# Optimization experiments

Measured on AMD Instinct MI355X. Metric: run time of the kernel, lower is better.

The kernel has to match this reference:

```python
import jax, jax.numpy as jnp
import numpy as np

KSZ = 1  # kernel_size from init_kwargs


def setup_inputs() -> dict:
    key = jax.random.key(0)
    k1, k2 = jax.random.split(key)
    S, B, H, W = 10, 8, 512, 512
    predicted = jax.random.normal(k1, (S, B, H, W), dtype=jnp.float32)
    target = jax.random.uniform(k2, (B, S, H, W), dtype=jnp.float32)
    mask = jnp.ones((B, S, H, W), dtype=jnp.float32)
    return {"predicted": predicted, "target": target, "mask": mask}


def reference(predicted, target, mask):
    # predicted: [S,B,H,W] -> [B,S,H,W] (torch .permute(1,0,2,3))
    pred = jnp.transpose(predicted, (1, 0, 2, 3))
    # use_weights=False -> weights = ones_like(target); mask unused
    weights = jnp.ones_like(target)
    H, W = target.shape[-2], target.shape[-1]

    # The torch loop does a running strict-< min over shifts (x,y) in row-major
    # order, seeded with the unshifted (0,0) loss. Final selection therefore is
    # the FIRST shift (in order [(0,0)] + loop order) achieving the global min,
    # which is exactly jnp.argmin's first-occurrence tie-breaking.
    shifts = [(0, 0)] + [(x, y) for x in range(-KSZ, KSZ + 1)
                         for y in range(-KSZ, KSZ + 1)]

    pad = jnp.pad(pred, ((0, 0), (0, 0), (KSZ, KSZ), (KSZ, KSZ)))
    valid = jnp.pad(jnp.ones((H, W), dtype=bool),
                    ((KSZ, KSZ), (KSZ, KSZ)))  # in-bounds map

    cands, losses = [], []
    for (x, y) in shifts:
        # candidate at pixel (i,j) is predicted[i+x, j+y]
        c = pad[..., KSZ + x:KSZ + x + H, KSZ + y:KSZ + y + W]
        v = valid[KSZ + x:KSZ + x + H, KSZ + y:KSZ + y + W]
        l = jnp.abs((target - c) * weights)
        losses.append(jnp.where(v, l, jnp.inf))
        cands.append(c)

    cands = jnp.stack(cands)    # [n_shifts, B, S, H, W]
    losses = jnp.stack(losses)  # [n_shifts, B, S, H, W]

    idx = jnp.argmin(losses, axis=0)                       # [B,S,H,W]
    kpred = jnp.take_along_axis(cands, idx[None], axis=0)[0]
    return jnp.transpose(kpred, (1, 0, 2, 3))  # back to [S,B,H,W]
```

## Files before the change

kernel.cpp:

```cpp
#include <hip/hip_runtime.h>

#define SS 10
#define BB 8
#define HH 512
#define WW 512
#define PLANE (HH * WW)
#define BIGV 3.0e38f

#define NBLK 2048
#define NITER 5

__global__ __launch_bounds__(256, 4) void shiftpred_kernel(
    const float* __restrict__ pred,
    const float* __restrict__ targ,
    float* __restrict__ out)
{
    int bid = blockIdx.x;
    int swz = (bid & 7) * (NBLK / 8) + (bid >> 3);

    int wv   = swz * 4 + (int)(threadIdx.x >> 6);
    int lane = (int)(threadIdx.x & 63);
    int h    = wv & (HH - 1);
    int sb0  = wv >> 9;
    int w0   = lane << 3;

    const bool hm_ok = (h > 0);
    const bool hp_ok = (h < HH - 1);
    const size_t roff  = (size_t)h * WW + w0;
    const size_t roffm = roff - WW;
    const size_t roffp = roff + WW;

    const float4 big4 = make_float4(BIGV, BIGV, BIGV, BIGV);

    auto tile_load = [&](int sb, float4& m0, float4& m1, float4& c0, float4& c1,
                         float4& p0, float4& p1, float4& t0, float4& t1) {
        int s = sb >> 3, b = sb & 7;
        const float* pp = pred + (size_t)sb * PLANE;
        const float* tp = targ + (size_t)(b * SS + s) * PLANE;
        c0 = *reinterpret_cast<const float4*>(pp + roff);
        c1 = *reinterpret_cast<const float4*>(pp + roff + 4);
        if (hm_ok) {
            m0 = *reinterpret_cast<const float4*>(pp + roffm);
            m1 = *reinterpret_cast<const float4*>(pp + roffm + 4);
        } else { m0 = big4; m1 = big4; }
        if (hp_ok) {
            p0 = *reinterpret_cast<const float4*>(pp + roffp);
            p1 = *reinterpret_cast<const float4*>(pp + roffp + 4);
        } else { p0 = big4; p1 = big4; }
        t0 = *reinterpret_cast<const float4*>(tp + roff);
        t1 = *reinterpret_cast<const float4*>(tp + roff + 4);
    };

    auto tile_compute = [&](int sb, float4 m0, float4 m1, float4 c0, float4 c1,
                            float4 p0, float4 p1, float4 t0, float4 t1) {
        float v[3][10];
        v[0][1] = m0.x; v[0][2] = m0.y; v[0][3] = m0.z; v[0][4] = m0.w;
        v[0][5] = m1.x; v[0][6] = m1.y; v[0][7] = m1.z; v[0][8] = m1.w;
        v[1][1] = c0.x; v[1][2] = c0.y; v[1][3] = c0.z; v[1][4] = c0.w;
        v[1][5] = c1.x; v[1][6] = c1.y; v[1][7] = c1.z; v[1][8] = c1.w;
        v[2][1] = p0.x; v[2][2] = p0.y; v[2][3] = p0.z; v[2][4] = p0.w;
        v[2][5] = p1.x; v[2][6] = p1.y; v[2][7] = p1.z; v[2][8] = p1.w;
        float lm = __shfl_up(m1.w, 1);  float rm = __shfl_down(m0.x, 1);
        float lc = __shfl_up(c1.w, 1);  float rc = __shfl_down(c0.x, 1);
        float lp = __shfl_up(p1.w, 1);  float rp = __shfl_down(p0.x, 1);
        bool e0 = (lane == 0), e63 = (lane == 63);
        v[0][0] = e0 ? BIGV : lm;  v[0][9] = e63 ? BIGV : rm;
        v[1][0] = e0 ? BIGV : lc;  v[1][9] = e63 ? BIGV : rc;
        v[2][0] = e0 ? BIGV : lp;  v[2][9] = e63 ? BIGV : rp;

        float tv[8]  = {t0.x, t0.y, t0.z, t0.w, t1.x, t1.y, t1.z, t1.w};
        float res[8];
        #pragma unroll
        for (int j = 0; j < 8; ++j) {
            float t = tv[j];
            float bestc = v[1][j + 1];
            float bestl = fabsf(t - bestc);
            #pragma unroll
            for (int xi = 0; xi < 3; ++xi) {
                #pragma unroll
                for (int yi = 0; yi < 3; ++yi) {
                    float c = v[xi][j + yi];
                    float l = fabsf(t - c);
                    if (l < bestl) { bestl = l; bestc = c; }
                }
            }
            res[j] = bestc;
        }
        float* op = out + (size_t)sb * PLANE + roff;
        *reinterpret_cast<float4*>(op)     = make_float4(res[0], res[1], res[2], res[3]);
        *reinterpret_cast<float4*>(op + 4) = make_float4(res[4], res[5], res[6], res[7]);
    };

    float4 cm0, cm1, cc0, cc1, cp0, cp1, ct0, ct1;
    float4 nm0, nm1, nc0, nc1, np0, np1, nt0, nt1;

    tile_load(sb0, cm0, cm1, cc0, cc1, cp0, cp1, ct0, ct1);
    #pragma unroll
    for (int it = 0; it < NITER; ++it) {
        int sb = sb0 + (it << 4);
        if (it < NITER - 1)
            tile_load(sb0 + ((it + 1) << 4),
                      nm0, nm1, nc0, nc1, np0, np1, nt0, nt1);
        tile_compute(sb, cm0, cm1, cc0, cc1, cp0, cp1, ct0, ct1);
        cm0 = nm0; cm1 = nm1; cc0 = nc0; cc1 = nc1;
        cp0 = np0; cp1 = np1; ct0 = nt0; ct1 = nt1;
    }
}

extern "C" void kernel_launch(void* const* d_in, const int* in_sizes, int n_in,
                              void* d_out, int out_size, void* d_ws, size_t ws_size,
                              hipStream_t stream) {
    const float* pred = (const float*)d_in[0];
    const float* targ = (const float*)d_in[1];
    float* out = (float*)d_out;
    shiftpred_kernel<<<NBLK, 256, 0, stream>>>(pred, targ, out);
}
```

Measured before the change: 247.5 us.

## Process 8-row bands per wave with a sliding row window and nontemporal I/O

Each wavefront now owns an 8-row band of one plane instead of a single row across five planes. A rolling three-row register window means each new output row needs only one new pred row, so pred reads per output drop from three rows to about 1.25. Target loads and output stores now use nontemporal builtins to limit cache pollution. In exchange each wave runs a longer serial chain of dependent row steps with only one-ahead prefetch, and the grid shrinks to 1280 blocks, which could reduce memory-level parallelism.

New measurement: 271.2 us. 9.6% more time.

```diff
diff --git a/kernel.cpp b/kernel.cpp
--- a/kernel.cpp
+++ b/kernel.cpp
@@ -7,8 +7,12 @@
 #define PLANE (HH * WW)
 #define BIGV 3.0e38f
 
-#define NBLK 2048
-#define NITER 5
+#define RB 8
+#define NBANDS (HH / RB)
+#define NWAVES (SS * BB * NBANDS)
+#define NBLK (NWAVES / 4)
+
+typedef float f32x4 __attribute__((ext_vector_type(4)));
 
 __global__ __launch_bounds__(256, 4) void shiftpred_kernel(
     const float* __restrict__ pred,
@@ -20,55 +24,48 @@
 
     int wv   = swz * 4 + (int)(threadIdx.x >> 6);
     int lane = (int)(threadIdx.x & 63);
-    int h    = wv & (HH - 1);
-    int sb0  = wv >> 9;
+    int band = wv & (NBANDS - 1);
+    int sb   = wv >> 6;
+    int h0   = band * RB;
     int w0   = lane << 3;
 
-    const bool hm_ok = (h > 0);
-    const bool hp_ok = (h < HH - 1);
-    const size_t roff  = (size_t)h * WW + w0;
-    const size_t roffm = roff - WW;
-    const size_t roffp = roff + WW;
+    const float* pp = pred + (size_t)sb * PLANE + w0;
+    const float* tp = targ + (size_t)((sb & 7) * SS + (sb >> 3)) * PLANE + w0;
+    float*       op = out  + (size_t)sb * PLANE + w0;
 
-    const float4 big4 = make_float4(BIGV, BIGV, BIGV, BIGV);
+    const bool e0  = (lane == 0);
+    const bool e63 = (lane == 63);
 
-    auto tile_load = [&](int sb, float4& m0, float4& m1, float4& c0, float4& c1,
-                         float4& p0, float4& p1, float4& t0, float4& t1) {
-        int s = sb >> 3, b = sb & 7;
-        const float* pp = pred + (size_t)sb * PLANE;
-        const float* tp = targ + (size_t)(b * SS + s) * PLANE;
-        c0 = *reinterpret_cast<const float4*>(pp + roff);
-        c1 = *reinterpret_cast<const float4*>(pp + roff + 4);
-        if (hm_ok) {
-            m0 = *reinterpret_cast<const float4*>(pp + roffm);
-            m1 = *reinterpret_cast<const float4*>(pp + roffm + 4);
-        } else { m0 = big4; m1 = big4; }
-        if (hp_ok) {
-            p0 = *reinterpret_cast<const float4*>(pp + roffp);
-            p1 = *reinterpret_cast<const float4*>(pp + roffp + 4);
-        } else { p0 = big4; p1 = big4; }
-        t0 = *reinterpret_cast<const float4*>(tp + roff);
-        t1 = *reinterpret_cast<const float4*>(tp + roff + 4);
+    auto ldp = [&](int hr, f32x4& q0, f32x4& q1, bool valid) {
+        if (valid) {
+            q0 = *reinterpret_cast<const f32x4*>(pp + (size_t)hr * WW);
+            q1 = *reinterpret_cast<const f32x4*>(pp + (size_t)hr * WW + 4);
+        } else { q0 = BIGV; q1 = BIGV; }
+    };
+    auto ldt = [&](int hr, f32x4& q0, f32x4& q1) {
+        q0 = __builtin_nontemporal_load(
+                 reinterpret_cast<const f32x4*>(tp + (size_t)hr * WW));
+        q1 = __builtin_nontemporal_load(
+                 reinterpret_cast<const f32x4*>(tp + (size_t)hr * WW + 4));
     };
 
-    auto tile_compute = [&](int sb, float4 m0, float4 m1, float4 c0, float4 c1,
-                            float4 p0, float4 p1, float4 t0, float4 t1) {
+    auto docompute = [&](int h, f32x4 a0, f32x4 a1, f32x4 b0, f32x4 b1,
+                         f32x4 c0, f32x4 c1, f32x4 t0, f32x4 t1) {
         float v[3][10];
-        v[0][1] = m0.x; v[0][2] = m0.y; v[0][3] = m0.z; v[0][4] = m0.w;
-        v[0][5] = m1.x; v[0][6] = m1.y; v[0][7] = m1.z; v[0][8] = m1.w;
-        v[1][1] = c0.x; v[1][2] = c0.y; v[1][3] = c0.z; v[1][4] = c0.w;
-        v[1][5] = c1.x; v[1][6] = c1.y; v[1][7] = c1.z; v[1][8] = c1.w;
-        v[2][1] = p0.x; v[2][2] = p0.y; v[2][3] = p0.z; v[2][4] = p0.w;
-        v[2][5] = p1.x; v[2][6] = p1.y; v[2][7] = p1.z; v[2][8] = p1.w;
-        float lm = __shfl_up(m1.w, 1);  float rm = __shfl_down(m0.x, 1);
-        float lc = __shfl_up(c1.w, 1);  float rc = __shfl_down(c0.x, 1);
-        float lp = __shfl_up(p1.w, 1);  float rp = __shfl_down(p0.x, 1);
-        bool e0 = (lane == 0), e63 = (lane == 63);
-        v[0][0] = e0 ? BIGV : lm;  v[0][9] = e63 ? BIGV : rm;
-        v[1][0] = e0 ? BIGV : lc;  v[1][9] = e63 ? BIGV : rc;
-        v[2][0] = e0 ? BIGV : lp;  v[2][9] = e63 ? BIGV : rp;
+        #pragma unroll
+        for (int k = 0; k < 4; ++k) {
+            v[0][1 + k] = a0[k]; v[0][5 + k] = a1[k];
+            v[1][1 + k] = b0[k]; v[1][5 + k] = b1[k];
+            v[2][1 + k] = c0[k]; v[2][5 + k] = c1[k];
+        }
+        float la = __shfl_up(a1[3], 1), ra = __shfl_down(a0[0], 1);
+        float lb = __shfl_up(b1[3], 1), rb = __shfl_down(b0[0], 1);
+        float lc = __shfl_up(c1[3], 1), rc = __shfl_down(c0[0], 1);
+        v[0][0] = e0 ? BIGV : la;  v[0][9] = e63 ? BIGV : ra;
+        v[1][0] = e0 ? BIGV : lb;  v[1][9] = e63 ? BIGV : rb;
+        v[2][0] = e0 ? BIGV : lc;  v[2][9] = e63 ? BIGV : rc;
 
-        float tv[8]  = {t0.x, t0.y, t0.z, t0.w, t1.x, t1.y, t1.z, t1.w};
+        float tv[8] = {t0[0], t0[1], t0[2], t0[3], t1[0], t1[1], t1[2], t1[3]};
         float res[8];
         #pragma unroll
         for (int j = 0; j < 8; ++j) {
@@ -86,24 +83,31 @@
             }
             res[j] = bestc;
         }
-        float* op = out + (size_t)sb * PLANE + roff;
-        *reinterpret_cast<float4*>(op)     = make_float4(res[0], res[1], res[2], res[3]);
-        *reinterpret_cast<float4*>(op + 4) = make_float4(res[4], res[5], res[6], res[7]);
+        f32x4 o0 = {res[0], res[1], res[2], res[3]};
+        f32x4 o1 = {res[4], res[5], res[6], res[7]};
+        __builtin_nontemporal_store(o0, reinterpret_cast<f32x4*>(op + (size_t)h * WW));
+        __builtin_nontemporal_store(o1, reinterpret_cast<f32x4*>(op + (size_t)h * WW + 4));
     };
 
-    float4 cm0, cm1, cc0, cc1, cp0, cp1, ct0, ct1;
-    float4 nm0, nm1, nc0, nc1, np0, np1, nt0, nt1;
+    f32x4 a0, a1, b0, b1, c0, c1, t0, t1;
+    f32x4 n0, n1, u0, u1;
 
-    tile_load(sb0, cm0, cm1, cc0, cc1, cp0, cp1, ct0, ct1);
+    ldp(h0 - 1, a0, a1, h0 > 0);
+    ldp(h0,     b0, b1, true);
+    ldp(h0 + 1, c0, c1, true);
+    ldt(h0,     t0, t1);
+
     #pragma unroll
-    for (int it = 0; it < NITER; ++it) {
-        int sb = sb0 + (it << 4);
-        if (it < NITER - 1)
-            tile_load(sb0 + ((it + 1) << 4),
-                      nm0, nm1, nc0, nc1, np0, np1, nt0, nt1);
-        tile_compute(sb, cm0, cm1, cc0, cc1, cp0, cp1, ct0, ct1);
-        cm0 = nm0; cm1 = nm1; cc0 = nc0; cc1 = nc1;
-        cp0 = np0; cp1 = np1; ct0 = nt0; ct1 = nt1;
+    for (int i = 0; i < RB; ++i) {
+        if (i < RB - 1) {
+            ldp(h0 + i + 2, n0, n1, (h0 + i + 2) < HH);
+            ldt(h0 + i + 1, u0, u1);
+        }
+        docompute(h0 + i, a0, a1, b0, b1, c0, c1, t0, t1);
+        if (i < RB - 1) {
+            a0 = b0; a1 = b1; b0 = c0; b1 = c1;
+            c0 = n0; c1 = n1; t0 = u0; t1 = u1;
+        }
     }
 }
 
```
